# Kernel optimization log

Measured on AMD Instinct MI355X. Metric: run time of the kernel, lower is better.

Reference implementation:

```python
import jax, jax.numpy as jnp
import numpy as np

B, H, L, D = 4, 16, 2048, 64
TOPK = 128


def setup_inputs() -> dict:
    key = jax.random.key(0)
    k1, k2, k3 = jax.random.split(key, 3)
    Q = jax.random.normal(k1, (B, H, L, D), dtype=jnp.float32)
    K = jax.random.normal(k2, (B, H, L, D), dtype=jnp.float32)
    V = jax.random.normal(k3, (B, H, L, D), dtype=jnp.float32)
    return {"Q": Q, "K": K, "V": V, "topk": TOPK}


def reference(Q, K, V, topk):
    # activation = softmax(d**-0.5 * x), as the docstring prescribes for vanilla attention
    scale = Q.shape[-1] ** -0.5
    neg = -jnp.finfo(Q.dtype).max  # max_neg_value, matching torch
    b, h, lq, d = Q.shape
    lk = K.shape[-2]

    # dots: [B,H,Lq,Lk]
    dots = jnp.einsum('bhqd,bhkd->bhqk', Q, K)
    # causal masking (True entries masked)
    causal = jnp.triu(jnp.ones((lq, lk), dtype=bool), 1)
    dots = jnp.where(causal, neg, dots)

    # top-k sparsification along keys
    top_dots, top_inds = jax.lax.top_k(dots, topk)          # [B,H,Lq,k]
    top_attn = jax.nn.softmax(top_dots * scale, axis=-1)    # activation on top values only

    # scatter activated values back into a zeroed [B,H,Lq,Lk] attention matrix
    bi = jnp.arange(b)[:, None, None, None]
    hi = jnp.arange(h)[None, :, None, None]
    qi = jnp.arange(lq)[None, None, :, None]
    attn = jnp.zeros_like(dots).at[bi, hi, qi, top_inds].set(top_attn)

    # out = attn @ V : [B,H,Lq,Dv]
    return jnp.einsum('bhqk,bhkd->bhqd', attn, V)
```

## Files before the change

### kernel.cpp

```cpp
#include <hip/hip_runtime.h>
#include <float.h>
#include <stdint.h>

#define QB        16
#define NTHREADS  512
#define LQ        2048
#define NDIM      64
#define KSEL      128
#define CHK       512
#define LDS_BYTES 53248
#define WS_NEEDED (2u * 8388608u * 2u)

typedef __attribute__((ext_vector_type(8))) short  s8v;
typedef __attribute__((ext_vector_type(4))) float  f32x4;

__device__ __forceinline__ unsigned ordf(float f) {
  unsigned u = __float_as_uint(f);
  return (u & 0x80000000u) ? ~u : (u | 0x80000000u);
}
__device__ __forceinline__ float unordf(unsigned u) {
  unsigned x = (u & 0x80000000u) ? (u & 0x7FFFFFFFu) : ~u;
  return __uint_as_float(x);
}
__device__ __forceinline__ unsigned short f2bf(float f) {
  unsigned u = __float_as_uint(f);
  return (unsigned short)((u + 0x7FFFu + ((u >> 16) & 1u)) >> 16);
}
__device__ __forceinline__ float bf2f(unsigned short h) {
  return __uint_as_float(((unsigned)h) << 16);
}

extern "C" __global__ void __launch_bounds__(256)
convert_k(const float4* __restrict__ K4, ushort4* __restrict__ Khi,
          ushort4* __restrict__ Klo) {
  const int idx = blockIdx.x * 256 + threadIdx.x;
  const float4 f = K4[idx];
  ushort4 h, l;
  h.x = f2bf(f.x); l.x = f2bf(f.x - bf2f(h.x));
  h.y = f2bf(f.y); l.y = f2bf(f.y - bf2f(h.y));
  h.z = f2bf(f.z); l.z = f2bf(f.z - bf2f(h.z));
  h.w = f2bf(f.w); l.w = f2bf(f.w - bf2f(h.w));
  Khi[idx] = h;
  Klo[idx] = l;
}

__device__ __forceinline__ void select_pv(
    const unsigned (&u)[32], const int g8, const int lane,
    int* __restrict__ list, float* __restrict__ wl,
    const float* __restrict__ Vg, float* __restrict__ outp) {
  const float C = 0.18033688011112042f;
  const unsigned long long ltmask = (1ull << lane) - 1ull;

  unsigned p = 0;
  int k = KSEL;
  bool exact = false;
#pragma unroll 1
  for (int b = 31; b >= 0; --b) {
    const unsigned T = p | (1u << b);
    int cnt = 0;
#pragma unroll
    for (int i8 = 0; i8 < 8; ++i8) {
      if (i8 <= g8) {
        cnt += (int)__popcll(__ballot(u[4 * i8 + 0] >= T));
        cnt += (int)__popcll(__ballot(u[4 * i8 + 1] >= T));
        cnt += (int)__popcll(__ballot(u[4 * i8 + 2] >= T));
        cnt += (int)__popcll(__ballot(u[4 * i8 + 3] >= T));
      }
    }
    if (cnt >= KSEL) {
      p = T;
      if (cnt == KSEL) { exact = true; break; }
    } else {
      k = KSEL - cnt;
    }
  }
  const unsigned tu   = exact ? (p - 1u) : p;
  const int      krem = exact ? 0 : k;
  const float    wt   = exact ? 0.f : exp2f(unordf(p) * C);

  float zacc = 0.f;
  int base = 0;
#pragma unroll
  for (int i8 = 0; i8 < 8; ++i8) {
    if (i8 > g8) break;
#pragma unroll
    for (int c4 = 0; c4 < 4; ++c4) {
      const unsigned ui = u[4 * i8 + c4];
      const unsigned long long bm = __ballot(ui > tu);
      if (ui > tu) {
        const int pos = base + (int)__popcll(bm & ltmask);
        const float wv = exp2f(unordf(ui) * C);
        list[pos] = i8 * 256 + (lane << 2) + c4;
        wl[pos]   = wv;
        zacc += wv;
      }
      base += (int)__popcll(bm);
    }
  }
  int n = base;
  if (wt > 0.f && krem > 0) {
    int carry = 0;
#pragma unroll
    for (int i8 = 0; i8 < 8; ++i8) {
      if (i8 > g8) break;
      const bool e0 = (u[4 * i8 + 0] == tu);
      const bool e1 = (u[4 * i8 + 1] == tu);
      const bool e2 = (u[4 * i8 + 2] == tu);
      const bool e3 = (u[4 * i8 + 3] == tu);
      const unsigned long long b0 = __ballot(e0);
      const unsigned long long b1 = __ballot(e1);
      const unsigned long long b2 = __ballot(e2);
      const unsigned long long b3 = __ballot(e3);
      int r = carry + (int)__popcll(b0 & ltmask) + (int)__popcll(b1 & ltmask) +
              (int)__popcll(b2 & ltmask) + (int)__popcll(b3 & ltmask);
      const int jb = i8 * 256 + (lane << 2);
      if (e0) { if (r < krem) { list[base + r] = jb + 0; wl[base + r] = wt; zacc += wt; } ++r; }
      if (e1) { if (r < krem) { list[base + r] = jb + 1; wl[base + r] = wt; zacc += wt; } ++r; }
      if (e2) { if (r < krem) { list[base + r] = jb + 2; wl[base + r] = wt; zacc += wt; } ++r; }
      if (e3) { if (r < krem) { list[base + r] = jb + 3; wl[base + r] = wt; zacc += wt; } ++r; }
      carry += (int)__popcll(b0) + (int)__popcll(b1) +
               (int)__popcll(b2) + (int)__popcll(b3);
      if (carry >= krem) break;
    }
    n = base + krem;
  }
  float Z = zacc;
#pragma unroll
  for (int off = 1; off < 64; off <<= 1) Z += __shfl_xor(Z, off, 64);
  __threadfence_block();

  float accv = 0.f;
  int i = 0;
  for (; i + 16 <= n; i += 16) {
    int4   jv[4];
    float4 wv[4];
#pragma unroll
    for (int g = 0; g < 4; ++g) {
      jv[g] = *(const int4*)  &list[i + 4 * g];
      wv[g] = *(const float4*)&wl[i + 4 * g];
    }
    float v[16];
#pragma unroll
    for (int g = 0; g < 4; ++g) {
      v[4 * g + 0] = Vg[(size_t)jv[g].x * NDIM + lane];
      v[4 * g + 1] = Vg[(size_t)jv[g].y * NDIM + lane];
      v[4 * g + 2] = Vg[(size_t)jv[g].z * NDIM + lane];
      v[4 * g + 3] = Vg[(size_t)jv[g].w * NDIM + lane];
    }
#pragma unroll
    for (int g = 0; g < 4; ++g)
      accv += wv[g].x * v[4 * g + 0] + wv[g].y * v[4 * g + 1] +
              wv[g].z * v[4 * g + 2] + wv[g].w * v[4 * g + 3];
  }
  for (; i < n; ++i) {
    accv += wl[i] * Vg[(size_t)list[i] * NDIM + lane];
  }
  *outp = accv / Z;
}

extern "C" __global__ void __launch_bounds__(NTHREADS, 4)
topk_attn_mfma(const float* __restrict__ Qg_, const float* __restrict__ Vg_,
               const unsigned short* __restrict__ Khi_,
               const unsigned short* __restrict__ Klo_,
               float* __restrict__ Out) {
  extern __shared__ char lds[];
  float*          s_chunk = (float*)(lds);
  unsigned short* qs_hi   = (unsigned short*)(lds + 32768);
  unsigned short* qs_lo   = (unsigned short*)(lds + 34816);
  int*            lists   = (int*)(lds + 36864);
  float*          wlist   = (float*)(lds + 45056);

  const int id  = blockIdx.x;
  const int xcd = id & 7;
  const int w   = id >> 3;
  const int bh  = w >> 4;
  const int qb  = ((w & 15) << 3) + xcd;

  const int q0   = qb * QB;
  const int tid  = threadIdx.x;
  const int lane = tid & 63;
  const int wid  = tid >> 6;
  const int m16  = lane & 15;
  const int quad = lane >> 4;

  const float* Qg  = Qg_ + ((size_t)(bh * LQ + q0)) * NDIM;
  const float* Vg  = Vg_ + ((size_t)bh) * LQ * NDIM;
  const unsigned short* Khi = Khi_ + ((size_t)bh) * LQ * NDIM;
  const unsigned short* Klo = Klo_ + ((size_t)bh) * LQ * NDIM;

#pragma unroll
  for (int e = tid; e < QB * NDIM; e += NTHREADS) {
    const float f = Qg[e];
    const unsigned short hh = f2bf(f);
    qs_hi[e] = hh;
    qs_lo[e] = f2bf(f - bf2f(hh));
  }
  __syncthreads();

  const unsigned short* qh = qs_hi + m16 * NDIM + quad * 8;
  const unsigned short* ql = qs_lo + m16 * NDIM + quad * 8;
  const s8v Ah0 = *(const s8v*)qh;
  const s8v Ah1 = *(const s8v*)(qh + 32);
  const s8v Al0 = *(const s8v*)ql;
  const s8v Al1 = *(const s8v*)(ql + 32);

  const int g8  = qb >> 4;
  const int nch = (qb >> 5) + 1;

  unsigned u0[32], u1[32];
#pragma unroll
  for (int i = 0; i < 32; ++i) { u0[i] = 0u; u1[i] = 0u; }

#pragma unroll
  for (int ch = 0; ch < 4; ++ch) {
    if (ch >= nch) break;
#pragma unroll 1
    for (int t = 0; t < 4; ++t) {
      const int jt  = (ch << 5) + wid + (t << 3);
      const int jc  = (jt << 4) + m16;
      const int jcl = jc - ch * CHK;
      if (jt > qb) {
#pragma unroll
        for (int reg = 0; reg < 4; ++reg)
          s_chunk[(quad * 4 + reg) * CHK + jcl] = -FLT_MAX;
        continue;
      }
      const unsigned short* kh = Khi + (size_t)jc * NDIM + quad * 8;
      const unsigned short* kl = Klo + (size_t)jc * NDIM + quad * 8;
      const s8v Bh0 = *(const s8v*)kh;
      const s8v Bh1 = *(const s8v*)(kh + 32);
      const s8v Bl0 = *(const s8v*)kl;
      const s8v Bl1 = *(const s8v*)(kl + 32);
      f32x4 c = {0.f, 0.f, 0.f, 0.f};
      c = __builtin_amdgcn_mfma_f32_16x16x32_bf16(Ah0, Bh0, c, 0, 0, 0);
      c = __builtin_amdgcn_mfma_f32_16x16x32_bf16(Ah1, Bh1, c, 0, 0, 0);
      c = __builtin_amdgcn_mfma_f32_16x16x32_bf16(Ah0, Bl0, c, 0, 0, 0);
      c = __builtin_amdgcn_mfma_f32_16x16x32_bf16(Ah1, Bl1, c, 0, 0, 0);
      c = __builtin_amdgcn_mfma_f32_16x16x32_bf16(Al0, Bh0, c, 0, 0, 0);
      c = __builtin_amdgcn_mfma_f32_16x16x32_bf16(Al1, Bh1, c, 0, 0, 0);
#pragma unroll
      for (int reg = 0; reg < 4; ++reg) {
        const int r = quad * 4 + reg;
        s_chunk[r * CHK + jcl] = (jc <= q0 + r) ? c[reg] : -FLT_MAX;
      }
    }
    __syncthreads();
    {
      const float4* rowA = (const float4*)(s_chunk + wid * CHK);
      const float4* rowB = (const float4*)(s_chunk + (wid + 8) * CHK);
#pragma unroll
      for (int hf = 0; hf < 2; ++hf) {
        const int i8 = 2 * ch + hf;
        if (i8 <= g8) {
          const float4 a = rowA[(hf << 6) + lane];
          u0[4 * i8 + 0] = ordf(a.x);
          u0[4 * i8 + 1] = ordf(a.y);
          u0[4 * i8 + 2] = ordf(a.z);
          u0[4 * i8 + 3] = ordf(a.w);
          const float4 b = rowB[(hf << 6) + lane];
          u1[4 * i8 + 0] = ordf(b.x);
          u1[4 * i8 + 1] = ordf(b.y);
          u1[4 * i8 + 2] = ordf(b.z);
          u1[4 * i8 + 3] = ordf(b.w);
        }
      }
    }
    __syncthreads();
  }

  select_pv(u0, g8, lane, lists + wid * KSEL, wlist + wid * KSEL, Vg,
            Out + ((size_t)(bh * LQ + q0 + wid)) * NDIM + lane);
  select_pv(u1, g8, lane, lists + (wid + 8) * KSEL, wlist + (wid + 8) * KSEL, Vg,
            Out + ((size_t)(bh * LQ + q0 + wid + 8)) * NDIM + lane);
}

#define FB_QB        8
#define FB_LDS_BYTES 73760

extern "C" __global__ void __launch_bounds__(NTHREADS, 4)
topk_attn_fb(const float* __restrict__ Qg_, const float* __restrict__ Kg_,
             const float* __restrict__ Vg_, float* __restrict__ Out) {
  extern __shared__ char lds[];
  float* s_phys = (float*)(lds);
  int*   lists  = (int*)(lds + 65536);
  float* wlist  = (float*)(lds + 69632);
  float* qs     = (float*)(lds + 65536);

  const int id  = blockIdx.x;
  const int xcd = id & 7;
  const int w   = id >> 3;
  const int bh  = w >> 5;
  const int qb  = ((w & 31) << 3) + xcd;

  const int q0   = qb * FB_QB;
  const int tid  = threadIdx.x;
  const int lane = tid & 63;
  const int wid  = tid >> 6;

  const float* Qg = Qg_ + ((size_t)(bh * LQ + q0)) * NDIM;
  const float* Kg = Kg_ + ((size_t)bh) * LQ * NDIM;
  const float* Vg = Vg_ + ((size_t)bh) * LQ * NDIM;

  if (tid < FB_QB * NDIM / 4) ((float4*)qs)[tid] = ((const float4*)Qg)[tid];
  __syncthreads();

  const int tq   = tid >> 8;
  const int tk   = tid & 255;
  const int j0   = tk << 3;
  const int qmax = q0 + FB_QB - 1;
  const bool active = (j0 <= qmax);

  float acc[4][8];
#pragma unroll
  for (int i = 0; i < 4; ++i)
#pragma unroll
    for (int j = 0; j < 8; ++j) acc[i][j] = 0.f;

  if (active) {
    const float4* K4  = (const float4*)(Kg + (size_t)j0 * NDIM);
    const float4* qs4 = (const float4*)(qs + tq * 4 * NDIM);
#pragma unroll 1
    for (int d4 = 0; d4 < 16; ++d4) {
      float4 qv[4];
#pragma unroll
      for (int i = 0; i < 4; ++i) qv[i] = qs4[i * 16 + d4];
#pragma unroll
      for (int g = 0; g < 4; ++g) {
        const float4 k0 = K4[(2 * g + 0) * 16 + d4];
        const float4 k1 = K4[(2 * g + 1) * 16 + d4];
#pragma unroll
        for (int i = 0; i < 4; ++i) {
          acc[i][2 * g + 0] += qv[i].x * k0.x + qv[i].y * k0.y +
                               qv[i].z * k0.z + qv[i].w * k0.w;
          acc[i][2 * g + 1] += qv[i].x * k1.x + qv[i].y * k1.y +
                               qv[i].z * k1.z + qv[i].w * k1.w;
        }
      }
    }
  }
  __syncthreads();

#pragma unroll
  for (int i = 0; i < 4; ++i) {
    const int q = q0 + tq * 4 + i;
    float4* srow4 = (float4*)(s_phys + (tq * 4 + i) * LQ);
    float4 lo, hi;
    lo.x = (j0 + 0 <= q) ? acc[i][0] : -FLT_MAX;
    lo.y = (j0 + 1 <= q) ? acc[i][1] : -FLT_MAX;
    lo.z = (j0 + 2 <= q) ? acc[i][2] : -FLT_MAX;
    lo.w = (j0 + 3 <= q) ? acc[i][3] : -FLT_MAX;
    hi.x = (j0 + 4 <= q) ? acc[i][4] : -FLT_MAX;
    hi.y = (j0 + 5 <= q) ? acc[i][5] : -FLT_MAX;
    hi.z = (j0 + 6 <= q) ? acc[i][6] : -FLT_MAX;
    hi.w = (j0 + 7 <= q) ? acc[i][7] : -FLT_MAX;
    srow4[tk * 2 + 0] = lo;
    srow4[tk * 2 + 1] = hi;
  }
  __syncthreads();

  const float C = 0.18033688011112042f;
  const int qi = wid;
  const int q = q0 + qi;
  const float* srow = s_phys + qi * LQ;
  const float4* srow4 = (const float4*)srow;

  unsigned u[32];
#pragma unroll
  for (int i = 0; i < 8; ++i) {
    const float4 v = srow4[lane + (i << 6)];
    u[4 * i + 0] = ordf(v.x);
    u[4 * i + 1] = ordf(v.y);
    u[4 * i + 2] = ordf(v.z);
    u[4 * i + 3] = ordf(v.w);
  }

  unsigned p = 0;
  int k = KSEL;
#pragma unroll 1
  for (int b = 31; b >= 0; --b) {
    const unsigned T = p | (1u << b);
    int cnt = 0;
#pragma unroll
    for (int i = 0; i < 32; ++i)
      cnt += (int)__popcll(__ballot(u[i] >= T));
    if (cnt >= KSEL) p = T;
    else             k = KSEL - cnt;
  }
  const unsigned tu = p;
  const int krem = k;
  const float wt = exp2f(unordf(tu) * C);

  const unsigned long long ltmask = (1ull << lane) - 1ull;
  float zacc = 0.f;
  int myeq = 0;
  int base = 0;
#pragma unroll
  for (int i = 0; i < 32; ++i) {
    const unsigned ui = u[i];
    const unsigned long long b = __ballot(ui > tu);
    if (ui > tu) {
      const int pos = base + (int)__popcll(b & ltmask);
      const int j = ((i >> 2) << 8) + (lane << 2) + (i & 3);
      const float wv = exp2f(unordf(ui) * C);
      lists[qi * KSEL + pos] = j;
      wlist[qi * KSEL + pos] = wv;
      zacc += wv;
    }
    base += (int)__popcll(b);
    myeq += (ui == tu) ? 1 : 0;
  }
  int n = base;
  if (wt > 0.f) {
    int te = myeq;
#pragma unroll
    for (int off = 1; off < 64; off <<= 1) te += __shfl_xor(te, off, 64);
    if (te == krem) {
#pragma unroll
      for (int i = 0; i < 32; ++i) {
        const unsigned long long b = __ballot(u[i] == tu);
        if (u[i] == tu) {
          const int pos = base + (int)__popcll(b & ltmask);
          const int j = ((i >> 2) << 8) + (lane << 2) + (i & 3);
          lists[qi * KSEL + pos] = j;
          wlist[qi * KSEL + pos] = wt;
          zacc += wt;
        }
        base += (int)__popcll(b);
      }
      n = base;
    } else {
      if (lane == 0) {
        int taken = 0, pos = base;
        for (int j = 0; j < LQ && taken < krem; ++j) {
          if (ordf(srow[j]) == tu) {
            lists[qi * KSEL + pos] = j;
            wlist[qi * KSEL + pos] = wt;
            pos++; taken++;
          }
        }
        zacc += wt * (float)krem;
      }
      n = KSEL;
    }
  }
  float Z = zacc;
#pragma unroll
  for (int off = 1; off < 64; off <<= 1) Z += __shfl_xor(Z, off, 64);
  __threadfence_block();

  float accv = 0.f;
  int i = 0;
  for (; i + 8 <= n; i += 8) {
    const int4   ja = *(const int4*)  &lists[qi * KSEL + i];
    const int4   jb = *(const int4*)  &lists[qi * KSEL + i + 4];
    const float4 wa = *(const float4*)&wlist[qi * KSEL + i];
    const float4 wb = *(const float4*)&wlist[qi * KSEL + i + 4];
    const float v0 = Vg[(size_t)ja.x * NDIM + lane];
    const float v1 = Vg[(size_t)ja.y * NDIM + lane];
    const float v2 = Vg[(size_t)ja.z * NDIM + lane];
    const float v3 = Vg[(size_t)ja.w * NDIM + lane];
    const float v4 = Vg[(size_t)jb.x * NDIM + lane];
    const float v5 = Vg[(size_t)jb.y * NDIM + lane];
    const float v6 = Vg[(size_t)jb.z * NDIM + lane];
    const float v7 = Vg[(size_t)jb.w * NDIM + lane];
    accv += wa.x * v0 + wa.y * v1 + wa.z * v2 + wa.w * v3 +
            wb.x * v4 + wb.y * v5 + wb.z * v6 + wb.w * v7;
  }
  for (; i < n; ++i) {
    const int j = lists[qi * KSEL + i];
    accv += wlist[qi * KSEL + i] * Vg[(size_t)j * NDIM + lane];
  }
  Out[((size_t)(bh * LQ + q)) * NDIM + lane] = accv / Z;
}

extern "C" void kernel_launch(void* const* d_in, const int* in_sizes, int n_in,
                              void* d_out, int out_size, void* d_ws, size_t ws_size,
                              hipStream_t stream) {
  (void)in_sizes; (void)n_in; (void)out_size;
  const float* Q = (const float*)d_in[0];
  const float* K = (const float*)d_in[1];
  const float* V = (const float*)d_in[2];
  float* Out = (float*)d_out;

  if (ws_size >= WS_NEEDED) {
    ushort4* Khi = (ushort4*)d_ws;
    ushort4* Klo = (ushort4*)((char*)d_ws + 8388608u * 2u);
    convert_k<<<dim3(8192), 256, 0, stream>>>((const float4*)K, Khi, Klo);

    (void)hipFuncSetAttribute(reinterpret_cast<const void*>(&topk_attn_mfma),
                              hipFuncAttributeMaxDynamicSharedMemorySize, LDS_BYTES);
    topk_attn_mfma<<<dim3(8192), NTHREADS, LDS_BYTES, stream>>>(
        Q, V, (const unsigned short*)Khi, (const unsigned short*)Klo, Out);
  } else {
    (void)hipFuncSetAttribute(reinterpret_cast<const void*>(&topk_attn_fb),
                              hipFuncAttributeMaxDynamicSharedMemorySize, FB_LDS_BYTES);
    topk_attn_fb<<<dim3(16384), NTHREADS, FB_LDS_BYTES, stream>>>(Q, K, V, Out);
  }
}
```

Baseline: 878.1 us.

## Halve query block to 8 rows per block, one row per wave, padded LDS stride

Each block now handles 8 query rows instead of 16, so every wave owns a single row and keeps one 32-entry register array instead of two. The grid doubles and LDS use drops, and launch bounds move to 6 blocks per CU to raise occupancy. Causal masking is moved from the score write into the selection stage. Only tiles up to the block's last query are computed, and the score rows use a padded stride to reduce LDS bank conflicts. In exchange, the 16-wide MFMA tile is half wasted on zero-padded query rows, so K loads and MFMA work per query roughly double.

```diff
diff --git a/kernel.cpp b/kernel.cpp
--- a/kernel.cpp
+++ b/kernel.cpp
@@ -2,13 +2,14 @@
 #include <float.h>
 #include <stdint.h>
 
-#define QB        16
+#define QB        8
 #define NTHREADS  512
 #define LQ        2048
 #define NDIM      64
 #define KSEL      128
 #define CHK       512
-#define LDS_BYTES 53248
+#define SSTR      516
+#define LDS_BYTES 28800
 #define WS_NEEDED (2u * 8388608u * 2u)
 
 typedef __attribute__((ext_vector_type(8))) short  s8v;
@@ -158,23 +159,23 @@
   *outp = accv / Z;
 }
 
-extern "C" __global__ void __launch_bounds__(NTHREADS, 4)
+extern "C" __global__ void __launch_bounds__(NTHREADS, 6)
 topk_attn_mfma(const float* __restrict__ Qg_, const float* __restrict__ Vg_,
                const unsigned short* __restrict__ Khi_,
                const unsigned short* __restrict__ Klo_,
                float* __restrict__ Out) {
   extern __shared__ char lds[];
   float*          s_chunk = (float*)(lds);
-  unsigned short* qs_hi   = (unsigned short*)(lds + 32768);
-  unsigned short* qs_lo   = (unsigned short*)(lds + 34816);
-  int*            lists   = (int*)(lds + 36864);
-  float*          wlist   = (float*)(lds + 45056);
+  unsigned short* qs_hi   = (unsigned short*)(lds + 16512);
+  unsigned short* qs_lo   = (unsigned short*)(lds + 18560);
+  int*            lists   = (int*)(lds + 20608);
+  float*          wlist   = (float*)(lds + 24704);
 
   const int id  = blockIdx.x;
   const int xcd = id & 7;
   const int w   = id >> 3;
-  const int bh  = w >> 4;
-  const int qb  = ((w & 15) << 3) + xcd;
+  const int bh  = w >> 5;
+  const int qb  = ((w & 31) << 3) + xcd;
 
   const int q0   = qb * QB;
   const int tid  = threadIdx.x;
@@ -189,8 +190,9 @@
   const unsigned short* Klo = Klo_ + ((size_t)bh) * LQ * NDIM;
 
 #pragma unroll
-  for (int e = tid; e < QB * NDIM; e += NTHREADS) {
-    const float f = Qg[e];
+  for (int e = tid; e < 16 * NDIM; e += NTHREADS) {
+    const int r = e >> 6;
+    const float f = (r < QB) ? Qg[e] : 0.f;
     const unsigned short hh = f2bf(f);
     qs_hi[e] = hh;
     qs_lo[e] = f2bf(f - bf2f(hh));
@@ -204,27 +206,23 @@
   const s8v Al0 = *(const s8v*)ql;
   const s8v Al1 = *(const s8v*)(ql + 32);
 
-  const int g8  = qb >> 4;
-  const int nch = (qb >> 5) + 1;
-
-  unsigned u0[32], u1[32];
-#pragma unroll
-  for (int i = 0; i < 32; ++i) { u0[i] = 0u; u1[i] = 0u; }
+  const int q    = q0 + wid;
+  const int g8   = q >> 8;
+  const int qmax = q0 + QB - 1;
+  const int nt   = (qmax >> 4) + 1;
+  const int nch  = (qmax >> 9) + 1;
+
+  unsigned u[32];
 
 #pragma unroll
   for (int ch = 0; ch < 4; ++ch) {
     if (ch >= nch) break;
 #pragma unroll 1
     for (int t = 0; t < 4; ++t) {
-      const int jt  = (ch << 5) + wid + (t << 3);
+      const int jt = (ch << 5) + wid + (t << 3);
+      if (jt >= nt) continue;
       const int jc  = (jt << 4) + m16;
-      const int jcl = jc - ch * CHK;
-      if (jt > qb) {
-#pragma unroll
-        for (int reg = 0; reg < 4; ++reg)
-          s_chunk[(quad * 4 + reg) * CHK + jcl] = -FLT_MAX;
-        continue;
-      }
+      const int jcl = jc - (ch << 9);
       const unsigned short* kh = Khi + (size_t)jc * NDIM + quad * 8;
       const unsigned short* kl = Klo + (size_t)jc * NDIM + quad * 8;
       const s8v Bh0 = *(const s8v*)kh;
@@ -233,45 +231,40 @@
       const s8v Bl1 = *(const s8v*)(kl + 32);
       f32x4 c = {0.f, 0.f, 0.f, 0.f};
       c = __builtin_amdgcn_mfma_f32_16x16x32_bf16(Ah0, Bh0, c, 0, 0, 0);
+      c = __builtin_amdgcn_mfma_f32_16x16x32_bf16(Al0, Bh0, c, 0, 0, 0);
       c = __builtin_amdgcn_mfma_f32_16x16x32_bf16(Ah1, Bh1, c, 0, 0, 0);
+      c = __builtin_amdgcn_mfma_f32_16x16x32_bf16(Al1, Bh1, c, 0, 0, 0);
       c = __builtin_amdgcn_mfma_f32_16x16x32_bf16(Ah0, Bl0, c, 0, 0, 0);
       c = __builtin_amdgcn_mfma_f32_16x16x32_bf16(Ah1, Bl1, c, 0, 0, 0);
-      c = __builtin_amdgcn_mfma_f32_16x16x32_bf16(Al0, Bh0, c, 0, 0, 0);
-      c = __builtin_amdgcn_mfma_f32_16x16x32_bf16(Al1, Bh1, c, 0, 0, 0);
-#pragma unroll
-      for (int reg = 0; reg < 4; ++reg) {
-        const int r = quad * 4 + reg;
-        s_chunk[r * CHK + jcl] = (jc <= q0 + r) ? c[reg] : -FLT_MAX;
+      if (quad < 2) {
+#pragma unroll
+        for (int reg = 0; reg < 4; ++reg) {
+          const int r = quad * 4 + reg;
+          s_chunk[r * SSTR + jcl] = c[reg];
+        }
       }
     }
     __syncthreads();
     {
-      const float4* rowA = (const float4*)(s_chunk + wid * CHK);
-      const float4* rowB = (const float4*)(s_chunk + (wid + 8) * CHK);
+      const float4* row4 = (const float4*)(s_chunk + wid * SSTR);
 #pragma unroll
       for (int hf = 0; hf < 2; ++hf) {
         const int i8 = 2 * ch + hf;
         if (i8 <= g8) {
-          const float4 a = rowA[(hf << 6) + lane];
-          u0[4 * i8 + 0] = ordf(a.x);
-          u0[4 * i8 + 1] = ordf(a.y);
-          u0[4 * i8 + 2] = ordf(a.z);
-          u0[4 * i8 + 3] = ordf(a.w);
-          const float4 b = rowB[(hf << 6) + lane];
-          u1[4 * i8 + 0] = ordf(b.x);
-          u1[4 * i8 + 1] = ordf(b.y);
-          u1[4 * i8 + 2] = ordf(b.z);
-          u1[4 * i8 + 3] = ordf(b.w);
+          const float4 a = row4[(hf << 6) + lane];
+          const int jb = (i8 << 8) + (lane << 2);
+          u[4 * i8 + 0] = (jb + 0 <= q) ? ordf(a.x) : 0u;
+          u[4 * i8 + 1] = (jb + 1 <= q) ? ordf(a.y) : 0u;
+          u[4 * i8 + 2] = (jb + 2 <= q) ? ordf(a.z) : 0u;
+          u[4 * i8 + 3] = (jb + 3 <= q) ? ordf(a.w) : 0u;
         }
       }
     }
     __syncthreads();
   }
 
-  select_pv(u0, g8, lane, lists + wid * KSEL, wlist + wid * KSEL, Vg,
-            Out + ((size_t)(bh * LQ + q0 + wid)) * NDIM + lane);
-  select_pv(u1, g8, lane, lists + (wid + 8) * KSEL, wlist + (wid + 8) * KSEL, Vg,
-            Out + ((size_t)(bh * LQ + q0 + wid + 8)) * NDIM + lane);
+  select_pv(u, g8, lane, lists + wid * KSEL, wlist + wid * KSEL, Vg,
+            Out + ((size_t)(bh * LQ + q)) * NDIM + lane);
 }
 
 #define FB_QB        8
@@ -489,7 +482,7 @@
 
     (void)hipFuncSetAttribute(reinterpret_cast<const void*>(&topk_attn_mfma),
                               hipFuncAttributeMaxDynamicSharedMemorySize, LDS_BYTES);
-    topk_attn_mfma<<<dim3(8192), NTHREADS, LDS_BYTES, stream>>>(
+    topk_attn_mfma<<<dim3(16384), NTHREADS, LDS_BYTES, stream>>>(
         Q, V, (const unsigned short*)Khi, (const unsigned short*)Klo, Out);
   } else {
     (void)hipFuncSetAttribute(reinterpret_cast<const void*>(&topk_attn_fb),
```

New measurement: 914.1 us. 4.1% more time.
